# Performance work log

Hardware: AMD Instinct MI355X
Metric: run time of the kernel (lower is better)

## Reference

```python
import jax, jax.numpy as jnp
import numpy as np

N_NODES = 100000
N_EDGES = 1600000
N_CLASS = 26
HIDDEN = 128
K = 3  # TAGConv hops


def setup_inputs() -> dict:
    key = jax.random.key(0)
    ks = jax.random.split(key, 12)
    x = jax.random.normal(ks[0], (N_NODES, N_CLASS), dtype=jnp.float32)
    edge_index = jax.random.randint(ks[1], (2, N_EDGES), 0, N_NODES, dtype=jnp.int64)
    edge_weight = jax.random.uniform(ks[2], (N_EDGES,), dtype=jnp.float32)
    # Per-hop weights (K+1 hops incl. hop 0) for each of the 3 TAGConv layers.
    def lin(k, fan_in, fan_out):
        s = 1.0 / np.sqrt(fan_in)
        return jax.random.uniform(k, (K + 1, fan_in, fan_out), dtype=jnp.float32, minval=-s, maxval=s)
    W1 = lin(ks[3], N_CLASS, HIDDEN)
    b1 = jnp.zeros((HIDDEN,), dtype=jnp.float32)
    W2 = lin(ks[4], HIDDEN, HIDDEN)
    b2 = jnp.zeros((HIDDEN,), dtype=jnp.float32)
    W3 = lin(ks[5], HIDDEN, N_CLASS)
    b3 = jnp.zeros((N_CLASS,), dtype=jnp.float32)
    return {"x": x, "edge_index": edge_index, "edge_weight": edge_weight,
            "W1": W1, "b1": b1, "W2": W2, "b2": b2, "W3": W3, "b3": b3}


def _gcn_norm(edge_index, edge_weight, n):
    # symmetric normalization deg^-1/2 * w * deg^-1/2, no self loops (PyG TAGConv)
    row, col = edge_index[0], edge_index[1]
    deg = jax.ops.segment_sum(edge_weight, col, num_segments=n)
    dinv = jnp.where(deg > 0, jax.lax.rsqrt(jnp.maximum(deg, 1e-12)), 0.0)
    return dinv[row] * edge_weight * dinv[col]


def _tag_conv(x, row, col, norm, W, b, n):
    # out = sum_k W_k(x_k), x_0 = x, x_k = A_norm x_{k-1}
    out = x @ W[0]
    h = x
    for k in range(1, K + 1):
        h = jax.ops.segment_sum(norm[:, None] * h[row], col, num_segments=n)
        out = out + h @ W[k]
    return out + b


def reference(x, edge_index, edge_weight, W1, b1, W2, b2, W3, b3):
    n = x.shape[0]
    row, col = edge_index[0], edge_index[1]
    norm = _gcn_norm(edge_index, edge_weight, n)  # identical for all 3 layers
    h = jax.nn.elu(_tag_conv(x, row, col, norm, W1, b1, n))
    h = jax.nn.elu(_tag_conv(h, row, col, norm, W2, b2, n))
    return _tag_conv(h, row, col, norm, W3, b3, n)
```

## Files before the change

kernel.cpp:

```cpp
#include <hip/hip_runtime.h>

#define NCLS 26
#define HID 128
#define EPB 8192
#define MAXBK 512
#define BCAP 6016
typedef unsigned short ushort_t;
typedef unsigned int uint_t;
typedef unsigned long long u64;

typedef __bf16 bf16x8 __attribute__((ext_vector_type(8)));
typedef float f32x4 __attribute__((ext_vector_type(4)));
typedef unsigned int u32x4 __attribute__((ext_vector_type(4)));
typedef unsigned int u32x2 __attribute__((ext_vector_type(2)));

static __device__ __forceinline__ float b2f(ushort_t h) {
  return __uint_as_float(((uint_t)h) << 16);
}
static __device__ __forceinline__ ushort_t f2b(float f) {
  uint_t u = __float_as_uint(f);
  uint_t r = (u + 0x7fffu + ((u >> 16) & 1u)) >> 16;
  return (ushort_t)r;
}
static __device__ __forceinline__ uint_t pack2(float f0, float f1) {
  return (uint_t)f2b(f0) | ((uint_t)f2b(f1) << 16);
}
static __device__ __forceinline__ float lo16(uint_t v) { return b2f((ushort_t)(v & 0xffffu)); }
static __device__ __forceinline__ float hi16(uint_t v) { return b2f((ushort_t)(v >> 16)); }
static __device__ __forceinline__ bf16x8 ld_frag(const ushort_t* p) {
  u32x4 v = *reinterpret_cast<const u32x4*>(p);
  return __builtin_bit_cast(bf16x8, v);
}


__global__ __launch_bounds__(256) void bucket_place(
    const int* __restrict__ ei, const float* __restrict__ ew,
    int* __restrict__ gcur, u64* __restrict__ bkt, int E, int nbk) {
  __shared__ uint_t lc[MAXBK];
  __shared__ uint_t lb[MAXBK];
  int tid = threadIdx.x;
  for (int t = tid; t < nbk; t += 256) lc[t] = 0;
  __syncthreads();
  int e0 = blockIdx.x * EPB;
#pragma unroll
  for (int i = 0; i < EPB / 256; ++i) {
    int e = e0 + tid + i * 256;
    if (e < E) atomicAdd(&lc[(uint_t)ei[E + e] >> 8], 1u);
  }
  __syncthreads();
  for (int t = tid; t < nbk; t += 256) {
    uint_t c = lc[t];
    lb[t] = c ? (uint_t)t * BCAP + (uint_t)atomicAdd(&gcur[t], (int)c) : 0u;
    lc[t] = 0;
  }
  __syncthreads();
#pragma unroll
  for (int i = 0; i < EPB / 256; ++i) {
    int e = e0 + tid + i * 256;
    if (e < E) {
      uint_t r = (uint_t)ei[e];
      uint_t c = (uint_t)ei[E + e];
      uint_t b = c >> 8;
      uint_t pos = lb[b] + atomicAdd(&lc[b], 1u);
      bkt[pos] = ((u64)(r | ((c & 255u) << 24)) << 32) | (u64)__float_as_uint(ew[e]);
    }
  }
}

__global__ void scan_buckets(const int* __restrict__ gcur, int* __restrict__ mbase,
                             int nbk, int E) {
  __shared__ int s[512];
  int t = threadIdx.x;
  int v = (t < nbk) ? gcur[t] : 0;
  s[t] = v;
  __syncthreads();
  for (int off = 1; off < 512; off <<= 1) {
    int u = (t >= off) ? s[t - off] : 0;
    __syncthreads();
    s[t] += u;
    __syncthreads();
  }
  if (t < nbk) mbase[t] = s[t] - v;
  if (t == 0) mbase[nbk] = E;
}

__global__ __launch_bounds__(256) void bucket_stats(
    const u64* __restrict__ bkt, const int* __restrict__ gcur, const int* __restrict__ mbase,
    int* __restrict__ start, float* __restrict__ dinv, int n, int E) {
  int b = blockIdx.x;
  __shared__ uint_t cnt[256];
  __shared__ float deg[256];
  __shared__ int ssc[256];
  int tid = threadIdx.x;
  cnt[tid] = 0;
  deg[tid] = 0.f;
  __syncthreads();
  int fill = gcur[b];
  const u64* w = bkt + (size_t)b * BCAP;
  for (int p = tid; p < fill; p += 256) {
    u64 v = w[p];
    uint_t cl = (uint_t)(v >> 56);
    float wv = __uint_as_float((uint_t)(v & 0xffffffffULL));
    atomicAdd(&cnt[cl], 1u);
    atomicAdd(&deg[cl], wv);
  }
  __syncthreads();
  int v0 = (int)cnt[tid];
  ssc[tid] = v0;
  __syncthreads();
  for (int off = 1; off < 256; off <<= 1) {
    int u = (tid >= off) ? ssc[tid - off] : 0;
    __syncthreads();
    ssc[tid] += u;
    __syncthreads();
  }
  int node = (b << 8) + tid;
  if (node < n) {
    start[node] = mbase[b] + ssc[tid] - v0;
    float d = deg[tid];
    dinv[node] = d > 0.f ? rsqrtf(fmaxf(d, 1e-12f)) : 0.f;
  }
  if (b == 0 && tid == 0) start[n] = E;
}

__global__ __launch_bounds__(256) void bucket_emit(
    const u64* __restrict__ bkt, const int* __restrict__ gcur, const int* __restrict__ start,
    const float* __restrict__ dinv, u32x2* __restrict__ meta, int n) {
  int b = blockIdx.x;
  __shared__ uint_t lcur[256];
  int tid = threadIdx.x;
  lcur[tid] = 0;
  __syncthreads();
  int fill = gcur[b];
  const u64* w = bkt + (size_t)b * BCAP;
  for (int p = tid; p < fill; p += 256) {
    u64 v = w[p];
    uint_t hi = (uint_t)(v >> 32);
    uint_t r = hi & 0xffffffu;
    uint_t cl = hi >> 24;
    float wv = __uint_as_float((uint_t)(v & 0xffffffffULL));
    uint_t node = ((uint_t)b << 8) + cl;
    float nrm = dinv[r] * wv * dinv[node];
    uint_t slot = (uint_t)start[node] + atomicAdd(&lcur[cl], 1u);
    u32x2 m;
    m.x = r;
    m.y = __float_as_uint(nrm);
    meta[slot] = m;
  }
}

__global__ __launch_bounds__(256) void prep_misc(
    const float* __restrict__ x, uint_t* __restrict__ x32,
    const float* __restrict__ W1, ushort_t* __restrict__ Wz1,
    const float* __restrict__ W2, ushort_t* __restrict__ Wz2,
    const float* __restrict__ W3, ushort_t* __restrict__ Wz3, int n, int gconv) {
  int blk = blockIdx.x;
  int tid = threadIdx.x;
  if (blk < gconv) {
    int idx = blk * 256 + tid;
    if (idx >= n * 16) return;
    int node = idx >> 4, lane = idx & 15;
    float f0 = 0.f, f1 = 0.f;
    if (lane < 13) {
      f0 = x[node * 26 + 2 * lane];
      f1 = x[node * 26 + 2 * lane + 1];
    }
    x32[idx] = pack2(f0, f1);
  } else if (blk < gconv + 64) {
    int idx = (blk - gconv) * 256 + tid;
    int i = idx & 7, l = (idx >> 3) & 63, j = (idx >> 9) & 7, t = idx >> 12;
    int k = 8 * (l >> 4) + i;
    int col = 16 * j + (l & 15);
    float v = (k < NCLS) ? W1[((size_t)t * NCLS + k) * 128 + col] : 0.f;
    Wz1[idx] = f2b(v);
  } else if (blk < gconv + 64 + 256) {
    int idx = (blk - gconv - 64) * 256 + tid;
    int i = idx & 7, l = (idx >> 3) & 63, j = (idx >> 9) & 7, t = idx >> 12;
    int s = t >> 2, tt = t & 3;
    int k = tt * 32 + 8 * (l >> 4) + i;
    int col = 16 * j + (l & 15);
    float v = W2[((size_t)s * HID + k) * 128 + col];
    Wz2[idx] = f2b(v);
  } else {
    int idx = (blk - gconv - 64 - 256) * 256 + tid;
    int i = idx & 7, l = (idx >> 3) & 63, j = (idx >> 9) & 7, t = idx >> 12;
    int k = t * 32 + 8 * (l >> 4) + i;
    int col = 16 * j + (l & 15);
    int s = col >> 5, c = col & 31;
    float v = (c < 26) ? W3[((size_t)s * 128 + k) * 26 + c] : 0.f;
    Wz3[idx] = f2b(v);
  }
}


__global__ __launch_bounds__(256) void spmm128_bf(
    const u32x2* __restrict__ meta, const int* __restrict__ start,
    const uint_t* __restrict__ in, uint_t* __restrict__ out, int n) {
  int node = blockIdx.x * 4 + (threadIdx.x >> 6);
  int lane = threadIdx.x & 63;
  if (node >= n) return;
  int s = start[node], m = start[node + 1] - s;
  int eq = lane >> 4;
  uint_t foff = (uint_t)(lane & 15) << 4;
  const char* inb = (const char*)in;
  float a0 = 0.f, a1 = 0.f, a2 = 0.f, a3 = 0.f, a4 = 0.f, a5 = 0.f, a6 = 0.f, a7 = 0.f;
  if (m > 0) {
    int i0 = eq, i1 = 4 + eq;
    u32x2 mt0 = meta[s + (i0 < m ? i0 : m - 1)];
    u32x2 mt1 = meta[s + (i1 < m ? i1 : m - 1)];
    for (int base = 0; base < m; base += 8) {
      int p0 = base + 8 + eq, p1 = base + 12 + eq;
      u32x2 nx0 = meta[s + (p0 < m ? p0 : m - 1)];
      u32x2 nx1 = meta[s + (p1 < m ? p1 : m - 1)];
      float w0 = (base + eq < m) ? __uint_as_float(mt0.y) : 0.f;
      float w1 = (base + 4 + eq < m) ? __uint_as_float(mt1.y) : 0.f;
      u32x4 v0 = *reinterpret_cast<const u32x4*>(inb + (((uint_t)mt0.x << 8) + foff));
      u32x4 v1 = *reinterpret_cast<const u32x4*>(inb + (((uint_t)mt1.x << 8) + foff));
      a0 += w0 * lo16(v0.x); a1 += w0 * hi16(v0.x);
      a2 += w0 * lo16(v0.y); a3 += w0 * hi16(v0.y);
      a4 += w0 * lo16(v0.z); a5 += w0 * hi16(v0.z);
      a6 += w0 * lo16(v0.w); a7 += w0 * hi16(v0.w);
      a0 += w1 * lo16(v1.x); a1 += w1 * hi16(v1.x);
      a2 += w1 * lo16(v1.y); a3 += w1 * hi16(v1.y);
      a4 += w1 * lo16(v1.z); a5 += w1 * hi16(v1.z);
      a6 += w1 * lo16(v1.w); a7 += w1 * hi16(v1.w);
      mt0 = nx0;
      mt1 = nx1;
    }
  }
  a0 += __shfl_xor(a0, 16); a1 += __shfl_xor(a1, 16);
  a2 += __shfl_xor(a2, 16); a3 += __shfl_xor(a3, 16);
  a4 += __shfl_xor(a4, 16); a5 += __shfl_xor(a5, 16);
  a6 += __shfl_xor(a6, 16); a7 += __shfl_xor(a7, 16);
  a0 += __shfl_xor(a0, 32); a1 += __shfl_xor(a1, 32);
  a2 += __shfl_xor(a2, 32); a3 += __shfl_xor(a3, 32);
  a4 += __shfl_xor(a4, 32); a5 += __shfl_xor(a5, 32);
  a6 += __shfl_xor(a6, 32); a7 += __shfl_xor(a7, 32);
  if (eq == 0) {
    u32x4 o;
    o.x = pack2(a0, a1);
    o.y = pack2(a2, a3);
    o.z = pack2(a4, a5);
    o.w = pack2(a6, a7);
    *reinterpret_cast<u32x4*>(out + (size_t)node * 64 + (foff >> 2)) = o;
  }
}

__global__ __launch_bounds__(256) void spmm26_bf(
    const u32x2* __restrict__ meta, const int* __restrict__ start,
    const uint_t* __restrict__ in, const uint_t* __restrict__ add,
    uint_t* __restrict__ out, int n) {
  int node = blockIdx.x * 32 + (threadIdx.x >> 3);
  int ln = threadIdx.x & 7;
  if (node >= n) return;
  int s = start[node], m = start[node + 1] - s;
  uint_t foff = (uint_t)ln << 3;
  const char* inb = (const char*)in;
  float a0 = 0.f, a1 = 0.f, a2 = 0.f, a3 = 0.f;
  if (m > 0) {
    for (int base = 0; base < m; base += 8) {
      int j = base + ln;
      u32x2 mt = meta[s + (j < m ? j : m - 1)];
      int rr = (int)mt.x;
      float ww = (j < m) ? __uint_as_float(mt.y) : 0.f;
#pragma unroll
      for (int k = 0; k < 8; ++k) {
        uint_t r = (uint_t)__shfl(rr, k, 8);
        float wv = __shfl(ww, k, 8);
        u32x2 v = *reinterpret_cast<const u32x2*>(inb + ((r << 6) + foff));
        a0 += wv * lo16(v.x); a1 += wv * hi16(v.x);
        a2 += wv * lo16(v.y); a3 += wv * hi16(v.y);
      }
    }
  }
  if (add) {
    u32x2 v = *reinterpret_cast<const u32x2*>(add + (size_t)node * 16 + 2 * ln);
    a0 += lo16(v.x); a1 += hi16(v.x);
    a2 += lo16(v.y); a3 += hi16(v.y);
  }
  u32x2 o;
  o.x = pack2(a0, a1);
  o.y = pack2(a2, a3);
  *reinterpret_cast<u32x2*>(out + (size_t)node * 16 + 2 * ln) = o;
}

__global__ __launch_bounds__(256) void spmm26_addf(
    const u32x2* __restrict__ meta, const int* __restrict__ start,
    const uint_t* __restrict__ in, float* __restrict__ out, int n) {
  int node = blockIdx.x * 32 + (threadIdx.x >> 3);
  int ln = threadIdx.x & 7;
  if (node >= n) return;
  int s = start[node], m = start[node + 1] - s;
  uint_t foff = (uint_t)ln << 3;
  const char* inb = (const char*)in;
  float a0 = 0.f, a1 = 0.f, a2 = 0.f, a3 = 0.f;
  if (m > 0) {
    for (int base = 0; base < m; base += 8) {
      int j = base + ln;
      u32x2 mt = meta[s + (j < m ? j : m - 1)];
      int rr = (int)mt.x;
      float ww = (j < m) ? __uint_as_float(mt.y) : 0.f;
#pragma unroll
      for (int k = 0; k < 8; ++k) {
        uint_t r = (uint_t)__shfl(rr, k, 8);
        float wv = __shfl(ww, k, 8);
        u32x2 v = *reinterpret_cast<const u32x2*>(inb + ((r << 6) + foff));
        a0 += wv * lo16(v.x); a1 += wv * hi16(v.x);
        a2 += wv * lo16(v.y); a3 += wv * hi16(v.y);
      }
    }
  }
  int c0 = 4 * ln;
  if (c0 + 0 < 26) out[(size_t)node * 26 + c0 + 0] += a0;
  if (c0 + 1 < 26) out[(size_t)node * 26 + c0 + 1] += a1;
  if (c0 + 2 < 26) out[(size_t)node * 26 + c0 + 2] += a2;
  if (c0 + 3 < 26) out[(size_t)node * 26 + c0 + 3] += a3;
}

template <int KW, int NSRC, int EPI, int MR, int GROUP>
__global__ __launch_bounds__(256) void mfma_gemm(
    const ushort_t* __restrict__ A0, const ushort_t* __restrict__ A1,
    const ushort_t* __restrict__ A2, const ushort_t* __restrict__ A3,
    const ushort_t* __restrict__ Wswz, const float* __restrict__ bias,
    ushort_t* __restrict__ outb, float* __restrict__ outf, int n) {
  constexpr int KSPS = KW / 32;
  constexpr int KSTEPS = NSRC * KSPS;
  constexpr int NGROUPS = KSTEPS / GROUP;
  __shared__ ushort_t sW[GROUP * 4096];
  const int tid = threadIdx.x;
  const int w = tid >> 6;
  const int l = tid & 63;
  const int row0 = blockIdx.x * (64 * MR) + w * (16 * MR);
  const int koff = 8 * (l >> 4);

  f32x4 acc[MR][8];
#pragma unroll
  for (int f = 0; f < MR; ++f)
#pragma unroll
    for (int j = 0; j < 8; ++j) acc[f][j] = (f32x4){0.f, 0.f, 0.f, 0.f};

  const ushort_t* const srcs[4] = {A0, A1, A2, A3};

  u32x4 gw[2 * GROUP];
#pragma unroll
  for (int c = 0; c < GROUP; ++c) {
    const ushort_t* p = Wswz + (size_t)c * 4096 + tid * 8;
    gw[2 * c] = *reinterpret_cast<const u32x4*>(p);
    gw[2 * c + 1] = *reinterpret_cast<const u32x4*>(p + 2048);
  }

#pragma unroll
  for (int g = 0; g < NGROUPS; ++g) {
    __syncthreads();
#pragma unroll
    for (int c = 0; c < GROUP; ++c) {
      *reinterpret_cast<u32x4*>(sW + c * 4096 + tid * 8) = gw[2 * c];
      *reinterpret_cast<u32x4*>(sW + c * 4096 + tid * 8 + 2048) = gw[2 * c + 1];
    }
    if (g + 1 < NGROUPS) {
#pragma unroll
      for (int c = 0; c < GROUP; ++c) {
        const ushort_t* p = Wswz + (size_t)(g + 1) * GROUP * 4096 + (size_t)c * 4096 + tid * 8;
        gw[2 * c] = *reinterpret_cast<const u32x4*>(p);
        gw[2 * c + 1] = *reinterpret_cast<const u32x4*>(p + 2048);
      }
    }
    __syncthreads();
#pragma unroll
    for (int tg = 0; tg < GROUP; ++tg) {
      const int t = g * GROUP + tg;
      const int s = t / KSPS;
      const int tt = t - s * KSPS;
      bf16x8 af[MR];
#pragma unroll
      for (int f = 0; f < MR; ++f) {
        int arow = row0 + f * 16 + (l & 15);
        int arow_c = arow < n ? arow : (n - 1);
        af[f] = ld_frag(srcs[s] + (size_t)arow_c * KW + tt * 32 + koff);
      }
      const ushort_t* wp = sW + tg * 4096 + l * 8;
#pragma unroll
      for (int j = 0; j < 8; ++j) {
        bf16x8 bfr = ld_frag(wp + j * 64 * 8);
#pragma unroll
        for (int f = 0; f < MR; ++f)
          acc[f][j] = __builtin_amdgcn_mfma_f32_16x16x32_bf16(af[f], bfr, acc[f][j], 0, 0, 0);
      }
    }
  }

  const int ccol = l & 15;
#pragma unroll
  for (int f = 0; f < MR; ++f) {
    const int crow0 = row0 + f * 16 + 4 * (l >> 4);
#pragma unroll
    for (int j = 0; j < 8; ++j) {
      if (EPI == 0) {
        int col = 16 * j + ccol;
        float bi = bias[col];
#pragma unroll
        for (int r = 0; r < 4; ++r) {
          int row = crow0 + r;
          if (row >= n) continue;
          float v = acc[f][j][r] + bi;
          v = v > 0.f ? v : (__expf(v) - 1.f);
          outb[(size_t)row * 128 + col] = f2b(v);
        }
      } else {
        int slot = j >> 1;
        int c = 16 * (j & 1) + ccol;
#pragma unroll
        for (int r = 0; r < 4; ++r) {
          int row = crow0 + r;
          if (row >= n) continue;
          float v = acc[f][j][r];
          if (slot == 0) {
            if (c < 26) outf[(size_t)row * 26 + c] = v + bias[c];
          } else {
            outb[((size_t)(slot - 1) * n + row) * 32 + c] = f2b(v);
          }
        }
      }
    }
  }
}


extern "C" void kernel_launch(void* const* d_in, const int* in_sizes, int n_in,
                              void* d_out, int out_size, void* d_ws, size_t ws_size,
                              hipStream_t stream) {
  const float* x  = (const float*)d_in[0];
  const int*   ei = (const int*)d_in[1];
  const float* ew = (const float*)d_in[2];
  const float* W1 = (const float*)d_in[3];
  const float* b1 = (const float*)d_in[4];
  const float* W2 = (const float*)d_in[5];
  const float* b2 = (const float*)d_in[6];
  const float* W3 = (const float*)d_in[7];
  const float* b3 = (const float*)d_in[8];
  float* out = (float*)d_out;

  const int n = in_sizes[0] / NCLS;
  const int E = in_sizes[2];
  const int nbk = (n + 255) >> 8;

  char* w = (char*)d_ws;
  auto alloc = [&](size_t bytes) {
    char* p = w;
    w += (bytes + 255) / 256 * 256;
    return p;
  };
  uint_t* H0 = (uint_t*)alloc((size_t)n * 64 * 4);
  uint_t* P1 = (uint_t*)alloc((size_t)n * 64 * 4);
  uint_t* P2 = (uint_t*)alloc((size_t)n * 64 * 4);
  uint_t* P3 = (uint_t*)alloc((size_t)n * 64 * 4);
  uint_t* H1 = (uint_t*)alloc((size_t)n * 64 * 4);
  uint_t* x32 = (uint_t*)alloc((size_t)n * 16 * 4);
  uint_t* q1  = (uint_t*)alloc((size_t)n * 16 * 4);
  uint_t* q2  = (uint_t*)alloc((size_t)n * 16 * 4);
  uint_t* q3  = (uint_t*)alloc((size_t)n * 16 * 4);
  uint_t* zb  = (uint_t*)alloc((size_t)n * 48 * 4);
  ushort_t* Wz1 = (ushort_t*)alloc(4 * 4096 * 2);
  ushort_t* Wz2 = (ushort_t*)alloc(16 * 4096 * 2);
  ushort_t* Wz3 = (ushort_t*)alloc(4 * 4096 * 2);
  u64*   bkt  = (u64*)zb;
  u32x2* meta = (u32x2*)alloc((size_t)E * 8);
  int*   start = (int*)alloc((size_t)(n + 1) * 4);
  float* dinv  = (float*)alloc((size_t)n * 4);
  int*   gcur  = (int*)alloc(MAXBK * 4);
  int*   mbase = (int*)alloc((MAXBK + 1) * 4);

  const int ab = (E + EPB - 1) / EPB;
  const int gconv = (n * 16 + 255) / 256;

  prep_misc<<<gconv + 64 + 256 + 64, 256, 0, stream>>>(x, x32, W1, Wz1, W2, Wz2, W3, Wz3,
                                                       n, gconv);

  hipMemsetAsync(gcur, 0, MAXBK * 4, stream);
  bucket_place<<<ab, 256, 0, stream>>>(ei, ew, gcur, bkt, E, nbk);
  scan_buckets<<<1, 512, 0, stream>>>(gcur, mbase, nbk, E);
  bucket_stats<<<nbk, 256, 0, stream>>>(bkt, gcur, mbase, start, dinv, n, E);
  bucket_emit<<<nbk, 256, 0, stream>>>(bkt, gcur, start, dinv, meta, n);

  const int g128 = (n + 3) / 4;
  const int g26  = (n + 31) / 32;
  const int gg1  = (n + 63) / 64;
  const int gg2  = (n + 127) / 128;

  spmm26_bf<<<g26, 256, 0, stream>>>(meta, start, x32, nullptr, q1, n);
  spmm26_bf<<<g26, 256, 0, stream>>>(meta, start, q1, nullptr, q2, n);
  spmm26_bf<<<g26, 256, 0, stream>>>(meta, start, q2, nullptr, q3, n);
  mfma_gemm<32, 4, 0, 1, 4><<<gg1, 256, 0, stream>>>(
      (const ushort_t*)x32, (const ushort_t*)q1, (const ushort_t*)q2, (const ushort_t*)q3,
      Wz1, b1, (ushort_t*)H0, nullptr, n);

  spmm128_bf<<<g128, 256, 0, stream>>>(meta, start, H0, P1, n);
  spmm128_bf<<<g128, 256, 0, stream>>>(meta, start, P1, P2, n);
  spmm128_bf<<<g128, 256, 0, stream>>>(meta, start, P2, P3, n);
  mfma_gemm<128, 4, 0, 2, 2><<<gg2, 256, 0, stream>>>(
      (const ushort_t*)H0, (const ushort_t*)P1, (const ushort_t*)P2, (const ushort_t*)P3,
      Wz2, b2, (ushort_t*)H1, nullptr, n);

  mfma_gemm<128, 1, 1, 1, 4><<<gg1, 256, 0, stream>>>(
      (const ushort_t*)H1, (const ushort_t*)H1, (const ushort_t*)H1, (const ushort_t*)H1,
      Wz3, b3, (ushort_t*)zb, out, n);

  uint_t* z1 = zb;
  uint_t* z2 = zb + (size_t)n * 16;
  uint_t* z3 = zb + (size_t)n * 32;
  spmm26_bf<<<g26, 256, 0, stream>>>(meta, start, z3, z2, q1, n);
  spmm26_bf<<<g26, 256, 0, stream>>>(meta, start, q1, z1, q2, n);
  spmm26_addf<<<g26, 256, 0, stream>>>(meta, start, q2, out, n);
}
```

Baseline: 462.9 us.

## Prefetch A fragments one group ahead and drop multi-row tiling in MFMA GEMM

The MFMA GEMM now loads the A-operand fragments for the next k-group into double-buffered registers while the current group runs its MFMAs, instead of loading them right before use. The MR row-tiling parameter is removed, so every GEMM uses 64-row blocks. The layer-2 GEMM moves from 128 rows per block with GROUP=2 to 64 rows per block with GROUP=4, which doubles the grid and reloads weights into shared memory more often. The goal is to hide global-load latency on the activation reads, at the cost of extra registers and less weight reuse per block.

```diff
diff --git a/kernel.cpp b/kernel.cpp
--- a/kernel.cpp
+++ b/kernel.cpp
@@ -317,7 +317,7 @@
   if (c0 + 3 < 26) out[(size_t)node * 26 + c0 + 3] += a3;
 }
 
-template <int KW, int NSRC, int EPI, int MR, int GROUP>
+template <int KW, int NSRC, int EPI, int GROUP>
 __global__ __launch_bounds__(256) void mfma_gemm(
     const ushort_t* __restrict__ A0, const ushort_t* __restrict__ A1,
     const ushort_t* __restrict__ A2, const ushort_t* __restrict__ A3,
@@ -330,17 +330,26 @@
   const int tid = threadIdx.x;
   const int w = tid >> 6;
   const int l = tid & 63;
-  const int row0 = blockIdx.x * (64 * MR) + w * (16 * MR);
+  const int row0 = blockIdx.x * 64 + w * 16;
   const int koff = 8 * (l >> 4);
-
-  f32x4 acc[MR][8];
-#pragma unroll
-  for (int f = 0; f < MR; ++f)
-#pragma unroll
-    for (int j = 0; j < 8; ++j) acc[f][j] = (f32x4){0.f, 0.f, 0.f, 0.f};
+  const int arow = row0 + (l & 15);
+  const int arow_c = arow < n ? arow : (n - 1);
+
+  f32x4 acc[8];
+#pragma unroll
+  for (int j = 0; j < 8; ++j) acc[j] = (f32x4){0.f, 0.f, 0.f, 0.f};
 
   const ushort_t* const srcs[4] = {A0, A1, A2, A3};
 
+  auto aload = [&](int t) {
+    const int s = t / KSPS;
+    const int tt = t - s * KSPS;
+    return ld_frag(srcs[s] + (size_t)arow_c * KW + tt * 32 + koff);
+  };
+
+  bf16x8 afA[GROUP], afB[GROUP];
+#pragma unroll
+  for (int c = 0; c < GROUP; ++c) afA[c] = aload(c);
   u32x4 gw[2 * GROUP];
 #pragma unroll
   for (int c = 0; c < GROUP; ++c) {
@@ -364,61 +373,54 @@
         gw[2 * c] = *reinterpret_cast<const u32x4*>(p);
         gw[2 * c + 1] = *reinterpret_cast<const u32x4*>(p + 2048);
       }
+#pragma unroll
+      for (int c = 0; c < GROUP; ++c) {
+        if (g & 1)
+          afA[c] = aload((g + 1) * GROUP + c);
+        else
+          afB[c] = aload((g + 1) * GROUP + c);
+      }
     }
     __syncthreads();
 #pragma unroll
     for (int tg = 0; tg < GROUP; ++tg) {
-      const int t = g * GROUP + tg;
-      const int s = t / KSPS;
-      const int tt = t - s * KSPS;
-      bf16x8 af[MR];
-#pragma unroll
-      for (int f = 0; f < MR; ++f) {
-        int arow = row0 + f * 16 + (l & 15);
-        int arow_c = arow < n ? arow : (n - 1);
-        af[f] = ld_frag(srcs[s] + (size_t)arow_c * KW + tt * 32 + koff);
-      }
+      bf16x8 af = (g & 1) ? afB[tg] : afA[tg];
       const ushort_t* wp = sW + tg * 4096 + l * 8;
 #pragma unroll
       for (int j = 0; j < 8; ++j) {
         bf16x8 bfr = ld_frag(wp + j * 64 * 8);
-#pragma unroll
-        for (int f = 0; f < MR; ++f)
-          acc[f][j] = __builtin_amdgcn_mfma_f32_16x16x32_bf16(af[f], bfr, acc[f][j], 0, 0, 0);
+        acc[j] = __builtin_amdgcn_mfma_f32_16x16x32_bf16(af, bfr, acc[j], 0, 0, 0);
       }
     }
   }
 
   const int ccol = l & 15;
-#pragma unroll
-  for (int f = 0; f < MR; ++f) {
-    const int crow0 = row0 + f * 16 + 4 * (l >> 4);
-#pragma unroll
-    for (int j = 0; j < 8; ++j) {
-      if (EPI == 0) {
-        int col = 16 * j + ccol;
-        float bi = bias[col];
-#pragma unroll
-        for (int r = 0; r < 4; ++r) {
-          int row = crow0 + r;
-          if (row >= n) continue;
-          float v = acc[f][j][r] + bi;
-          v = v > 0.f ? v : (__expf(v) - 1.f);
-          outb[(size_t)row * 128 + col] = f2b(v);
-        }
-      } else {
-        int slot = j >> 1;
-        int c = 16 * (j & 1) + ccol;
-#pragma unroll
-        for (int r = 0; r < 4; ++r) {
-          int row = crow0 + r;
-          if (row >= n) continue;
-          float v = acc[f][j][r];
-          if (slot == 0) {
-            if (c < 26) outf[(size_t)row * 26 + c] = v + bias[c];
-          } else {
-            outb[((size_t)(slot - 1) * n + row) * 32 + c] = f2b(v);
-          }
+  const int crow0 = row0 + 4 * (l >> 4);
+#pragma unroll
+  for (int j = 0; j < 8; ++j) {
+    if (EPI == 0) {
+      int col = 16 * j + ccol;
+      float bi = bias[col];
+#pragma unroll
+      for (int r = 0; r < 4; ++r) {
+        int row = crow0 + r;
+        if (row >= n) continue;
+        float v = acc[j][r] + bi;
+        v = v > 0.f ? v : (__expf(v) - 1.f);
+        outb[(size_t)row * 128 + col] = f2b(v);
+      }
+    } else {
+      int slot = j >> 1;
+      int c = 16 * (j & 1) + ccol;
+#pragma unroll
+      for (int r = 0; r < 4; ++r) {
+        int row = crow0 + r;
+        if (row >= n) continue;
+        float v = acc[j][r];
+        if (slot == 0) {
+          if (c < 26) outf[(size_t)row * 26 + c] = v + bias[c];
+        } else {
+          outb[((size_t)(slot - 1) * n + row) * 32 + c] = f2b(v);
         }
       }
     }
@@ -484,24 +486,23 @@
 
   const int g128 = (n + 3) / 4;
   const int g26  = (n + 31) / 32;
-  const int gg1  = (n + 63) / 64;
-  const int gg2  = (n + 127) / 128;
+  const int gg   = (n + 63) / 64;
 
   spmm26_bf<<<g26, 256, 0, stream>>>(meta, start, x32, nullptr, q1, n);
   spmm26_bf<<<g26, 256, 0, stream>>>(meta, start, q1, nullptr, q2, n);
   spmm26_bf<<<g26, 256, 0, stream>>>(meta, start, q2, nullptr, q3, n);
-  mfma_gemm<32, 4, 0, 1, 4><<<gg1, 256, 0, stream>>>(
+  mfma_gemm<32, 4, 0, 4><<<gg, 256, 0, stream>>>(
       (const ushort_t*)x32, (const ushort_t*)q1, (const ushort_t*)q2, (const ushort_t*)q3,
       Wz1, b1, (ushort_t*)H0, nullptr, n);
 
   spmm128_bf<<<g128, 256, 0, stream>>>(meta, start, H0, P1, n);
   spmm128_bf<<<g128, 256, 0, stream>>>(meta, start, P1, P2, n);
   spmm128_bf<<<g128, 256, 0, stream>>>(meta, start, P2, P3, n);
-  mfma_gemm<128, 4, 0, 2, 2><<<gg2, 256, 0, stream>>>(
+  mfma_gemm<128, 4, 0, 4><<<gg, 256, 0, stream>>>(
       (const ushort_t*)H0, (const ushort_t*)P1, (const ushort_t*)P2, (const ushort_t*)P3,
       Wz2, b2, (ushort_t*)H1, nullptr, n);
 
-  mfma_gemm<128, 1, 1, 1, 4><<<gg1, 256, 0, stream>>>(
+  mfma_gemm<128, 1, 1, 4><<<gg, 256, 0, stream>>>(
       (const ushort_t*)H1, (const ushort_t*)H1, (const ushort_t*)H1, (const ushort_t*)H1,
       Wz3, b3, (ushort_t*)zb, out, n);
 
```

Result: no change. 458.1 us (-1.0%).
